# Optimization experiments

Hardware: AMD Instinct MI355X
Metric: run time of the kernel (lower is better)

Reference implementation:

```python
import jax, jax.numpy as jnp
import numpy as np

B, S, D, H = 2, 2048, 1024, 16
HD = D // H
SCALE = HD ** -0.5

def setup_inputs() -> dict:
    key = jax.random.key(0)
    ks = jax.random.split(key, 3)
    x = jax.random.normal(ks[0], (B, S, D), dtype=jnp.float32)
    Wqkv = jax.random.normal(ks[1], (D, 3 * D), dtype=jnp.float32) * (D ** -0.5)
    bqkv = jnp.zeros((3 * D,), dtype=jnp.float32)
    Wproj = jax.random.normal(ks[2], (D, D), dtype=jnp.float32) * (D ** -0.5)
    bproj = jnp.zeros((D,), dtype=jnp.float32)
    return {"x": x, "Wqkv": Wqkv, "bqkv": bqkv, "Wproj": Wproj, "bproj": bproj}

def reference(x, Wqkv, bqkv, Wproj, bproj):
    b, s, d = x.shape
    qkv = x @ Wqkv + bqkv                       # (b, s, 3d)
    qkv = qkv.reshape(b, s, 3, H, HD)
    q, k, v = (qkv[:, :, 0], qkv[:, :, 1], qkv[:, :, 2])  # (b, s, h, hd)
    # scores: (b, h, s, s)
    attn = jnp.einsum('bqhd,bkhd->bhqk', q, k) * SCALE
    attn = jax.nn.softmax(attn, axis=-1)
    out = jnp.einsum('bhqk,bkhd->bqhd', attn, v).reshape(b, s, d)
    out = out @ Wproj + bproj
    return out
```

## Files before the change

kernel.cpp:

```cpp
#include <hip/hip_runtime.h>

typedef __attribute__((ext_vector_type(8))) short bf16x8;
typedef __attribute__((ext_vector_type(4))) float f32x4;
typedef __attribute__((ext_vector_type(16))) float f32x16;
typedef unsigned short u16;
typedef unsigned int u32;

#define MFMA16(a,b,c) __builtin_amdgcn_mfma_f32_16x16x32_bf16((a),(b),(c),0,0,0)
#define MFMA32(a,b,c) __builtin_amdgcn_mfma_f32_32x32x16_bf16((a),(b),(c),0,0,0)

#if __has_builtin(__builtin_amdgcn_exp2f)
#define EXP2(x) __builtin_amdgcn_exp2f(x)
#else
#define EXP2(x) __expf((x) * 0.6931471805599453f)
#endif

__device__ __forceinline__ u16 f2bf(float f) {
  u32 u = __builtin_bit_cast(u32, f);
  u += 0x7FFFu + ((u >> 16) & 1u);
  return (u16)(u >> 16);
}

__device__ __forceinline__ u32 cvtpk(float lo, float hi) {
  u32 r;
  asm("v_cvt_pk_bf16_f32 %0, %1, %2" : "=v"(r) : "v"(lo), "v"(hi));
  return r;
}

__device__ __forceinline__ void gload16(const u16* g, u16* l) {
  __builtin_amdgcn_global_load_lds(
      (const __attribute__((address_space(1))) u32*)(const void*)g,
      (__attribute__((address_space(3))) u32*)(void*)l, 16, 0, 0);
}

__device__ __forceinline__ bf16x8 ldsfrag(const u16* lds, int row, int chunk) {
  return *(const bf16x8*)(lds + row * 64 + ((chunk ^ (row & 7)) << 3));
}

__global__ __launch_bounds__(256) void convert_x(const float* __restrict__ in,
                                                 u16* __restrict__ out, int n4) {
  int i = blockIdx.x * blockDim.x + threadIdx.x;
  int stride = gridDim.x * blockDim.x;
  for (; i < n4; i += stride) {
    float4 v = ((const float4*)in)[i];
    u32 lo = (u32)f2bf(v.x) | ((u32)f2bf(v.y) << 16);
    u32 hi = (u32)f2bf(v.z) | ((u32)f2bf(v.w) << 16);
    uint2 pv; pv.x = lo; pv.y = hi;
    ((uint2*)out)[i] = pv;
  }
}

__global__ __launch_bounds__(256) void transpose_w(const float* __restrict__ in,
                                                   u16* __restrict__ out,
                                                   int R, int C) {
  __shared__ float t[32][33];
  int c0 = blockIdx.x * 32, r0 = blockIdx.y * 32;
  int tc = threadIdx.x & 31, tr = threadIdx.x >> 5;
#pragma unroll
  for (int j = 0; j < 4; ++j) {
    int r = tr + j * 8;
    t[r][tc] = in[(size_t)(r0 + r) * C + c0 + tc];
  }
  __syncthreads();
#pragma unroll
  for (int j = 0; j < 4; ++j) {
    int cc = tr + j * 8;
    out[(size_t)(c0 + cc) * R + r0 + tc] = f2bf(t[tc][cc]);
  }
}

template <int MODE>
__global__ __launch_bounds__(256, 3) void gemm_k(
    const u16* __restrict__ A, const u16* __restrict__ Bt,
    const float* __restrict__ bias,
    u16* __restrict__ Qo, u16* __restrict__ Ko, u16* __restrict__ Vt,
    float* __restrict__ Of) {
  __shared__ alignas(16) u16 As[3][4096];
  __shared__ alignas(16) u16 Bs[3][4096];
  const int tid = threadIdx.x;
  const int wid = tid >> 6, lane = tid & 63;
  const int g = lane >> 4, lr = lane & 15;
  const int m0 = blockIdx.y * 128, n0 = blockIdx.x * 128;
  const int wr = (wid >> 1) * 64, wc = (wid & 1) * 64;

  f32x4 acc[4][4];
#pragma unroll
  for (int i = 0; i < 4; ++i)
#pragma unroll
    for (int j = 0; j < 4; ++j) acc[i][j] = (f32x4){0.f, 0.f, 0.f, 0.f};

  const u16* Ab = A + (size_t)m0 * 1024;
  const u16* Bb = Bt + (size_t)n0 * 1024;

  const int srow = tid >> 2, sc = tid & 3;
  auto stage = [&](int buf, int kt) {
#pragma unroll
    for (int i = 0; i < 2; ++i) {
      int s = tid + i * 256;
      int row = srow + i * 64;
      gload16(Ab + (size_t)row * 1024 + kt + sc * 8, As[buf] + s * 8);
      gload16(Bb + (size_t)row * 1024 + kt + sc * 8, Bs[buf] + s * 8);
    }
  };

  stage(0, 0);
  stage(1, 32);
  int cur = 0;
  for (int ki = 0; ki < 32; ++ki) {
    if (ki + 2 < 32) {
      int nxt = cur + 2; if (nxt >= 3) nxt -= 3;
      stage(nxt, (ki + 2) * 32);
    }
    if (ki < 30)       asm volatile("s_waitcnt vmcnt(8)" ::: "memory");
    else if (ki == 30) asm volatile("s_waitcnt vmcnt(4)" ::: "memory");
    else               asm volatile("s_waitcnt vmcnt(0)" ::: "memory");
    __builtin_amdgcn_sched_barrier(0);
    __builtin_amdgcn_s_barrier();
    __builtin_amdgcn_sched_barrier(0);

    bf16x8 af[4], bfr[4];
#pragma unroll
    for (int i = 0; i < 4; ++i)
      af[i] = *(const bf16x8*)(As[cur] + (wr + i * 16 + lr) * 32 + g * 8);
#pragma unroll
    for (int j = 0; j < 4; ++j)
      bfr[j] = *(const bf16x8*)(Bs[cur] + (wc + j * 16 + lr) * 32 + g * 8);
    __builtin_amdgcn_s_setprio(1);
#pragma unroll
    for (int i = 0; i < 4; ++i)
#pragma unroll
      for (int j = 0; j < 4; ++j)
        acc[i][j] = MFMA16(af[i], bfr[j], acc[i][j]);
    __builtin_amdgcn_s_setprio(0);

    __builtin_amdgcn_s_barrier();
    __builtin_amdgcn_sched_barrier(0);
    cur += 1; if (cur >= 3) cur -= 3;
  }

  if constexpr (MODE == 1) {
#pragma unroll
    for (int i = 0; i < 4; ++i) {
      int row = m0 + wr + i * 16 + g * 4;
#pragma unroll
      for (int j = 0; j < 4; ++j) {
        int col = n0 + wc + j * 16 + lr;
        float bv = bias[col];
#pragma unroll
        for (int r = 0; r < 4; ++r)
          Of[(size_t)(row + r) * 1024 + col] = acc[i][j][r] + bv;
      }
    }
  } else {
    const int sel = n0 >> 10;
#pragma unroll
    for (int i = 0; i < 4; ++i) {
      int row = m0 + wr + i * 16 + g * 4;
      int b = row >> 11, s = row & 2047;
#pragma unroll
      for (int j = 0; j < 4; ++j) {
        int col = n0 + wc + j * 16 + lr;
        float bv = bias[col];
        int nn = col & 1023;
        int h = nn >> 6, hd = nn & 63;
        if (sel == 2) {
          u16 pk[4];
#pragma unroll
          for (int r = 0; r < 4; ++r) pk[r] = f2bf(acc[i][j][r] + bv);
          uint2 pv;
          pv.x = (u32)pk[0] | ((u32)pk[1] << 16);
          pv.y = (u32)pk[2] | ((u32)pk[3] << 16);
          *(uint2*)(Vt + (size_t)((b * 16 + h) * 64 + hd) * 2048 + s) = pv;
        } else {
          u16* dst = (sel == 0) ? Qo : Ko;
#pragma unroll
          for (int r = 0; r < 4; ++r)
            dst[(size_t)((b * 16 + h) * 2048 + s + r) * 64 + hd] =
                f2bf(acc[i][j][r] + bv);
        }
      }
    }
  }
}

__global__ __launch_bounds__(256, 2) void attn_k(const u16* __restrict__ Q,
                                                 const u16* __restrict__ K,
                                                 const u16* __restrict__ Vt,
                                                 u16* __restrict__ O) {
  __shared__ alignas(16) u16 Ks[3][4096];
  __shared__ alignas(16) u16 Vs[3][4096];
  __shared__ alignas(16) u32 Ps[4 * 1088];
  const int tid = threadIdx.x;
  const int wid = tid >> 6, lane = tid & 63;
  const int l31 = lane & 31, b5 = lane >> 5;
  const int p = blockIdx.x;
  const int l = (p & 7) * 64 + (p >> 3);
  const int qt = l & 15, bh = l >> 4;
  const u16* Qh = Q + (size_t)bh * 2048 * 64;
  const u16* Kh = K + (size_t)bh * 2048 * 64;
  const u16* Vh = Vt + (size_t)bh * 64 * 2048;

  const int qbase = qt * 128 + wid * 32;
  const u16* qp = Qh + (size_t)(qbase + l31) * 64 + b5 * 8;
  bf16x8 qf[4];
#pragma unroll
  for (int c = 0; c < 4; ++c) qf[c] = *(const bf16x8*)(qp + 16 * c);
  __builtin_amdgcn_sched_barrier(0);

  auto stage = [&](int buf, int t) {
#pragma unroll
    for (int i = 0; i < 2; ++i) {
      int s = tid + i * 256;
      int row = s >> 3, c = (s & 7) ^ (row & 7);
      gload16(Kh + (t * 64 + row) * 64 + c * 8, Ks[buf] + s * 8);
      gload16(Vh + row * 2048 + t * 64 + c * 8, Vs[buf] + s * 8);
    }
  };
  stage(0, 0);
  stage(1, 1);

  u32* pw = Ps + wid * 1088 + l31 * 34;

  f32x16 accO0, accO1;
#pragma unroll
  for (int r = 0; r < 16; ++r) { accO0[r] = 0.f; accO1[r] = 0.f; }
  float mraw = -1e30f;
  float mC = 0.f;
  float lsum = 0.f;

  const float C2 = 0.125f * 1.44269504088896f;

  int cur = 0;
  for (int t = 0; t < 32; ++t) {
    if (t + 2 < 32) {
      int nxt = cur + 2; if (nxt >= 3) nxt -= 3;
      stage(nxt, t + 2);
    }
    if (t < 30)       asm volatile("s_waitcnt vmcnt(8)" ::: "memory");
    else if (t == 30) asm volatile("s_waitcnt vmcnt(4)" ::: "memory");
    else              asm volatile("s_waitcnt vmcnt(0)" ::: "memory");
    __builtin_amdgcn_sched_barrier(0);
    __builtin_amdgcn_s_barrier();
    __builtin_amdgcn_sched_barrier(0);

    const u16* Kc = Ks[cur];
    const u16* Vc = Vs[cur];

    f32x16 s0, s1;
#pragma unroll
    for (int r = 0; r < 16; ++r) { s0[r] = 0.f; s1[r] = 0.f; }
    __builtin_amdgcn_s_setprio(1);
#pragma unroll
    for (int c = 0; c < 4; ++c) {
      bf16x8 k0 = ldsfrag(Kc, l31, 2 * c + b5);
      bf16x8 k1 = ldsfrag(Kc, 32 + l31, 2 * c + b5);
      s0 = MFMA32(k0, qf[c], s0);
      s1 = MFMA32(k1, qf[c], s1);
    }
    __builtin_amdgcn_s_setprio(0);

    float rmax;
    {
      float a0 = fmaxf(fmaxf(s0[0], s0[1]), fmaxf(s0[2], s0[3]));
      float a1 = fmaxf(fmaxf(s0[4], s0[5]), fmaxf(s0[6], s0[7]));
      float a2 = fmaxf(fmaxf(s0[8], s0[9]), fmaxf(s0[10], s0[11]));
      float a3 = fmaxf(fmaxf(s0[12], s0[13]), fmaxf(s0[14], s0[15]));
      float b0 = fmaxf(fmaxf(s1[0], s1[1]), fmaxf(s1[2], s1[3]));
      float b1 = fmaxf(fmaxf(s1[4], s1[5]), fmaxf(s1[6], s1[7]));
      float b2 = fmaxf(fmaxf(s1[8], s1[9]), fmaxf(s1[10], s1[11]));
      float b3 = fmaxf(fmaxf(s1[12], s1[13]), fmaxf(s1[14], s1[15]));
      rmax = fmaxf(fmaxf(fmaxf(a0, a1), fmaxf(a2, a3)),
                   fmaxf(fmaxf(b0, b1), fmaxf(b2, b3)));
    }
    rmax = fmaxf(rmax, __shfl_xor(rmax, 32));

    if (__any(rmax > mraw + 64.f)) {
      float mn = fmaxf(mraw, rmax);
      float al = EXP2((mraw - mn) * C2);
      mraw = mn;
      mC = mn * C2;
      lsum *= al;
#pragma unroll
      for (int r = 0; r < 16; ++r) {
        float ar = __shfl(al, (r & 3) + 8 * (r >> 2) + 4 * b5);
        accO0[r] *= ar;
        accO1[r] *= ar;
      }
    }

    u32 w0[8], w1[8];
#pragma unroll
    for (int i = 0; i < 8; ++i) {
      float p0 = EXP2(__builtin_fmaf(s0[2 * i], C2, -mC));
      float p1 = EXP2(__builtin_fmaf(s0[2 * i + 1], C2, -mC));
      float p2 = EXP2(__builtin_fmaf(s1[2 * i], C2, -mC));
      float p3 = EXP2(__builtin_fmaf(s1[2 * i + 1], C2, -mC));
      lsum += (p0 + p1) + (p2 + p3);
      w0[i] = cvtpk(p0, p1);
      w1[i] = cvtpk(p2, p3);
    }
#pragma unroll
    for (int j = 0; j < 4; ++j) {
      uint2 a; a.x = w0[2 * j]; a.y = w0[2 * j + 1];
      uint2 b; b.x = w1[2 * j]; b.y = w1[2 * j + 1];
      *(uint2*)(pw + 4 * j + 2 * b5) = a;
      *(uint2*)(pw + 16 + 4 * j + 2 * b5) = b;
    }

    __builtin_amdgcn_s_setprio(1);
#pragma unroll
    for (int c = 0; c < 4; ++c) {
      uint2 qa = *(const uint2*)(pw + 8 * c + 4 * b5);
      uint2 qb = *(const uint2*)(pw + 8 * c + 4 * b5 + 2);
      uint4 u; u.x = qa.x; u.y = qa.y; u.z = qb.x; u.w = qb.y;
      bf16x8 pf = __builtin_bit_cast(bf16x8, u);
      bf16x8 v0 = ldsfrag(Vc, l31, 2 * c + b5);
      bf16x8 v1 = ldsfrag(Vc, 32 + l31, 2 * c + b5);
      accO0 = MFMA32(pf, v0, accO0);
      accO1 = MFMA32(pf, v1, accO1);
    }
    __builtin_amdgcn_s_setprio(0);

    __builtin_amdgcn_s_barrier();
    __builtin_amdgcn_sched_barrier(0);
    cur += 1; if (cur >= 3) cur -= 3;
  }

  float ls = lsum + __shfl_xor(lsum, 32);
  float inv = 1.f / ls;
  const int b = bh >> 4, h = bh & 15;
#pragma unroll
  for (int r = 0; r < 16; ++r) {
    float ir = __shfl(inv, (r & 3) + 8 * (r >> 2) + 4 * b5);
    int qr = qbase + (r & 3) + 8 * (r >> 2) + 4 * b5;
    size_t rowoff = (size_t)(b * 2048 + qr) * 1024 + h * 64;
    O[rowoff + l31] = f2bf(accO0[r] * ir);
    O[rowoff + 32 + l31] = f2bf(accO1[r] * ir);
  }
}

extern "C" void kernel_launch(void* const* d_in, const int* in_sizes, int n_in,
                              void* d_out, int out_size, void* d_ws, size_t ws_size,
                              hipStream_t stream) {
  (void)in_sizes; (void)n_in; (void)out_size; (void)ws_size;
  const float* x = (const float*)d_in[0];
  const float* Wqkv = (const float*)d_in[1];
  const float* bqkv = (const float*)d_in[2];
  const float* Wproj = (const float*)d_in[3];
  const float* bproj = (const float*)d_in[4];
  float* out = (float*)d_out;

  char* ws = (char*)d_ws;
  size_t off = 0;
  auto alloc = [&](size_t bytes) {
    void* p = ws + off;
    off += (bytes + 255) & ~(size_t)255;
    return p;
  };
  u16* xb     = (u16*)alloc((size_t)4096 * 1024 * 2);
  u16* Wqkvt  = (u16*)alloc((size_t)3072 * 1024 * 2);
  u16* Wprojt = (u16*)alloc((size_t)1024 * 1024 * 2);
  u16* Qb     = (u16*)alloc((size_t)32 * 2048 * 64 * 2);
  u16* Kb     = (u16*)alloc((size_t)32 * 2048 * 64 * 2);
  u16* Vtb    = (u16*)alloc((size_t)32 * 64 * 2048 * 2);
  u16* AOb    = (u16*)alloc((size_t)4096 * 1024 * 2);

  convert_x<<<2048, 256, 0, stream>>>(x, xb, 4096 * 1024 / 4);
  transpose_w<<<dim3(96, 32), 256, 0, stream>>>(Wqkv, Wqkvt, 1024, 3072);
  transpose_w<<<dim3(32, 32), 256, 0, stream>>>(Wproj, Wprojt, 1024, 1024);
  gemm_k<0><<<dim3(24, 32), 256, 0, stream>>>(xb, Wqkvt, bqkv, Qb, Kb, Vtb, nullptr);
  attn_k<<<512, 256, 0, stream>>>(Qb, Kb, Vtb, AOb);
  gemm_k<1><<<dim3(8, 32), 256, 0, stream>>>(AOb, Wprojt, bproj, nullptr, nullptr, nullptr, out);
}
```

Baseline: 132.6 us.

## Keep P in registers via permlane32 swap and transposed PV MFMA; swizzle GEMM LDS

In attention, the softmax probabilities no longer round-trip through LDS. They are rearranged across lane halves with permlane32_swap and fed as the B operand of a transposed P·V MFMA. Because of this, output rows map to lanes, so the rescale and final normalisation drop their shuffles, and the output store becomes packed 8-byte writes. Separately, the GEMM LDS tiles get an XOR swizzle on the 16-byte chunk index to reduce bank conflicts on fragment reads. The main risks are correctness of the lane and fragment mapping and a less coalesced output store pattern.

```diff
diff --git a/kernel.cpp b/kernel.cpp
--- a/kernel.cpp
+++ b/kernel.cpp
@@ -25,6 +25,20 @@
   u32 r;
   asm("v_cvt_pk_bf16_f32 %0, %1, %2" : "=v"(r) : "v"(lo), "v"(hi));
   return r;
+}
+
+__device__ __forceinline__ void swap32(u32& a, u32& b) {
+#if __has_builtin(__builtin_amdgcn_permlane32_swap)
+  auto r = __builtin_amdgcn_permlane32_swap((int)a, (int)b, false, false);
+  a = (u32)r[0];
+  b = (u32)r[1];
+#else
+  u32 pa = __shfl_xor(a, 32), pb = __shfl_xor(b, 32);
+  bool lo = ((threadIdx.x & 32) == 0);
+  u32 na = lo ? a : pb;
+  u32 nb = lo ? pa : b;
+  a = na; b = nb;
+#endif
 }
 
 __device__ __forceinline__ void gload16(const u16* g, u16* l) {
@@ -98,8 +112,9 @@
     for (int i = 0; i < 2; ++i) {
       int s = tid + i * 256;
       int row = srow + i * 64;
-      gload16(Ab + (size_t)row * 1024 + kt + sc * 8, As[buf] + s * 8);
-      gload16(Bb + (size_t)row * 1024 + kt + sc * 8, Bs[buf] + s * 8);
+      int csrc = sc ^ ((row >> 1) & 3);
+      gload16(Ab + (size_t)row * 1024 + kt + csrc * 8, As[buf] + s * 8);
+      gload16(Bb + (size_t)row * 1024 + kt + csrc * 8, Bs[buf] + s * 8);
     }
   };
 
@@ -120,11 +135,17 @@
 
     bf16x8 af[4], bfr[4];
 #pragma unroll
-    for (int i = 0; i < 4; ++i)
-      af[i] = *(const bf16x8*)(As[cur] + (wr + i * 16 + lr) * 32 + g * 8);
-#pragma unroll
-    for (int j = 0; j < 4; ++j)
-      bfr[j] = *(const bf16x8*)(Bs[cur] + (wc + j * 16 + lr) * 32 + g * 8);
+    for (int i = 0; i < 4; ++i) {
+      int row = wr + i * 16 + lr;
+      int slot = g ^ ((row >> 1) & 3);
+      af[i] = *(const bf16x8*)(As[cur] + row * 32 + slot * 8);
+    }
+#pragma unroll
+    for (int j = 0; j < 4; ++j) {
+      int row = wc + j * 16 + lr;
+      int slot = g ^ ((row >> 1) & 3);
+      bfr[j] = *(const bf16x8*)(Bs[cur] + row * 32 + slot * 8);
+    }
     __builtin_amdgcn_s_setprio(1);
 #pragma unroll
     for (int i = 0; i < 4; ++i)
@@ -189,7 +210,6 @@
                                                  u16* __restrict__ O) {
   __shared__ alignas(16) u16 Ks[3][4096];
   __shared__ alignas(16) u16 Vs[3][4096];
-  __shared__ alignas(16) u32 Ps[4 * 1088];
   const int tid = threadIdx.x;
   const int wid = tid >> 6, lane = tid & 63;
   const int l31 = lane & 31, b5 = lane >> 5;
@@ -218,8 +238,6 @@
   };
   stage(0, 0);
   stage(1, 1);
-
-  u32* pw = Ps + wid * 1088 + l31 * 34;
 
   f32x16 accO0, accO1;
 #pragma unroll
@@ -282,9 +300,8 @@
       lsum *= al;
 #pragma unroll
       for (int r = 0; r < 16; ++r) {
-        float ar = __shfl(al, (r & 3) + 8 * (r >> 2) + 4 * b5);
-        accO0[r] *= ar;
-        accO1[r] *= ar;
+        accO0[r] *= al;
+        accO1[r] *= al;
       }
     }
 
@@ -299,25 +316,23 @@
       w0[i] = cvtpk(p0, p1);
       w1[i] = cvtpk(p2, p3);
     }
-#pragma unroll
-    for (int j = 0; j < 4; ++j) {
-      uint2 a; a.x = w0[2 * j]; a.y = w0[2 * j + 1];
-      uint2 b; b.x = w1[2 * j]; b.y = w1[2 * j + 1];
-      *(uint2*)(pw + 4 * j + 2 * b5) = a;
-      *(uint2*)(pw + 16 + 4 * j + 2 * b5) = b;
-    }
 
     __builtin_amdgcn_s_setprio(1);
 #pragma unroll
     for (int c = 0; c < 4; ++c) {
-      uint2 qa = *(const uint2*)(pw + 8 * c + 4 * b5);
-      uint2 qb = *(const uint2*)(pw + 8 * c + 4 * b5 + 2);
-      uint4 u; u.x = qa.x; u.y = qa.y; u.z = qb.x; u.w = qb.y;
+      u32 a0, a1, b0, b1;
+      if (c == 0)      { a0 = w0[0]; b0 = w0[2]; a1 = w0[1]; b1 = w0[3]; }
+      else if (c == 1) { a0 = w0[4]; b0 = w0[6]; a1 = w0[5]; b1 = w0[7]; }
+      else if (c == 2) { a0 = w1[0]; b0 = w1[2]; a1 = w1[1]; b1 = w1[3]; }
+      else             { a0 = w1[4]; b0 = w1[6]; a1 = w1[5]; b1 = w1[7]; }
+      swap32(a0, b0);
+      swap32(a1, b1);
+      uint4 u; u.x = a0; u.y = a1; u.z = b0; u.w = b1;
       bf16x8 pf = __builtin_bit_cast(bf16x8, u);
       bf16x8 v0 = ldsfrag(Vc, l31, 2 * c + b5);
       bf16x8 v1 = ldsfrag(Vc, 32 + l31, 2 * c + b5);
-      accO0 = MFMA32(pf, v0, accO0);
-      accO1 = MFMA32(pf, v1, accO1);
+      accO0 = MFMA32(v0, pf, accO0);
+      accO1 = MFMA32(v1, pf, accO1);
     }
     __builtin_amdgcn_s_setprio(0);
 
@@ -329,13 +344,17 @@
   float ls = lsum + __shfl_xor(lsum, 32);
   float inv = 1.f / ls;
   const int b = bh >> 4, h = bh & 15;
-#pragma unroll
-  for (int r = 0; r < 16; ++r) {
-    float ir = __shfl(inv, (r & 3) + 8 * (r >> 2) + 4 * b5);
-    int qr = qbase + (r & 3) + 8 * (r >> 2) + 4 * b5;
-    size_t rowoff = (size_t)(b * 2048 + qr) * 1024 + h * 64;
-    O[rowoff + l31] = f2bf(accO0[r] * ir);
-    O[rowoff + 32 + l31] = f2bf(accO1[r] * ir);
+  u16* orow = O + (size_t)(b * 2048 + qbase + l31) * 1024 + h * 64;
+#pragma unroll
+  for (int rg = 0; rg < 4; ++rg) {
+    int hd0 = 8 * rg + 4 * b5;
+    uint2 o0, o1;
+    o0.x = cvtpk(accO0[4 * rg + 0] * inv, accO0[4 * rg + 1] * inv);
+    o0.y = cvtpk(accO0[4 * rg + 2] * inv, accO0[4 * rg + 3] * inv);
+    o1.x = cvtpk(accO1[4 * rg + 0] * inv, accO1[4 * rg + 1] * inv);
+    o1.y = cvtpk(accO1[4 * rg + 2] * inv, accO1[4 * rg + 3] * inv);
+    *(uint2*)(orow + hd0) = o0;
+    *(uint2*)(orow + 32 + hd0) = o1;
   }
 }
 
```

After: 128.1 us. -3.4%, faster.
